# Performance work log

Measured on AMD Instinct MI355X. Metric: run time of the kernel, lower is better.

Reference implementation:

```python
import jax, jax.numpy as jnp
import numpy as np

STRIDES = (8, 16, 32, 64, 128)
SIZES = ((100, 160), (50, 80), (25, 40), (13, 20), (7, 10))  # 800x1280 image, P3-P7
NC = 80      # num_classes
C = 256      # head channels
NCONV = 4    # tower depth
N = 2        # batch
PRIOR_PROB = 0.01


def conv3x3(x, w, b):
    # x: [N,C,H,W], w: [O,I,3,3] -> [N,O,H,W], stride 1, SAME padding
    y = jax.lax.conv_general_dilated(x, w, (1, 1), 'SAME',
                                     dimension_numbers=('NCHW', 'OIHW', 'NCHW'))
    return y + b[None, :, None, None]


def group_norm(x, g, b, groups=32, eps=1e-5):
    n, c, h, w = x.shape
    xr = x.reshape(n, groups, c // groups, h, w)
    m = xr.mean((2, 3, 4), keepdims=True)
    v = ((xr - m) ** 2).mean((2, 3, 4), keepdims=True)
    xn = ((xr - m) * jax.lax.rsqrt(v + eps)).reshape(n, c, h, w)
    return xn * g[None, :, None, None] + b[None, :, None, None]


def setup_inputs() -> dict:
    key = jax.random.key(0)
    ks = iter(jax.random.split(key, 16))
    d = {}
    for l, (h, w) in enumerate(SIZES):
        d[f'feat{l}'] = jax.random.normal(next(ks), (N, C, h, w), jnp.float32)
    # torch init: conv weights ~ N(0, 0.01), biases 0, GN weight 1 / bias 0
    d['cls_w'] = jax.random.normal(next(ks), (NCONV, C, C, 3, 3), jnp.float32) * 0.01
    d['cls_b'] = jnp.zeros((NCONV, C), jnp.float32)
    d['cls_gw'] = jnp.ones((NCONV, C), jnp.float32)
    d['cls_gb'] = jnp.zeros((NCONV, C), jnp.float32)
    d['box_w'] = jax.random.normal(next(ks), (NCONV, C, C, 3, 3), jnp.float32) * 0.01
    d['box_b'] = jnp.zeros((NCONV, C), jnp.float32)
    d['box_gw'] = jnp.ones((NCONV, C), jnp.float32)
    d['box_gb'] = jnp.zeros((NCONV, C), jnp.float32)
    d['score_w'] = jax.random.normal(next(ks), (NC, C, 3, 3), jnp.float32) * 0.01
    bias_value = -np.log((1.0 - PRIOR_PROB) / PRIOR_PROB)
    d['score_b'] = jnp.full((NC,), bias_value, jnp.float32)
    d['pred_w'] = jax.random.normal(next(ks), (4, C, 3, 3), jnp.float32) * 0.01
    d['pred_b'] = jnp.zeros((4,), jnp.float32)
    d['ctr_w'] = jax.random.normal(next(ks), (1, C, 3, 3), jnp.float32) * 0.01
    d['ctr_b'] = jnp.zeros((1,), jnp.float32)
    d['scales'] = jnp.ones((5,), jnp.float32)
    return d


def reference(feat0, feat1, feat2, feat3, feat4,
              cls_w, cls_b, cls_gw, cls_gb,
              box_w, box_b, box_gw, box_gb,
              score_w, score_b, pred_w, pred_b, ctr_w, ctr_b, scales):
    feats = [feat0, feat1, feat2, feat3, feat4]
    outs = []
    for l, x in enumerate(feats):
        c = x
        r = x
        for i in range(NCONV):  # shared cls / bbox towers (conv -> GN -> ReLU)
            c = jax.nn.relu(group_norm(conv3x3(c, cls_w[i], cls_b[i]), cls_gw[i], cls_gb[i]))
            r = jax.nn.relu(group_norm(conv3x3(r, box_w[i], box_b[i]), box_gw[i], box_gb[i]))
        logits = conv3x3(c, score_w, score_b)                     # [N,K,H,W]
        ctr = conv3x3(r, ctr_w, ctr_b)                            # centerness_on_reg=True
        # norm_reg_targets=True: relu(scale * pred) * stride
        reg = jax.nn.relu(conv3x3(r, pred_w, pred_b) * scales[l]) * STRIDES[l]
        n, _, h, w = logits.shape
        logits = logits.transpose(0, 2, 3, 1).reshape(n, h * w, NC)
        ctr = ctr.transpose(0, 2, 3, 1).reshape(n, h * w, 1)
        reg = reg.transpose(0, 2, 3, 1).reshape(n, h * w, 4)
        # ShiftGenerator: grid of (x,y) centers at arange*stride (offset=0)
        sx = jnp.arange(w, dtype=jnp.float32) * STRIDES[l]
        sy = jnp.arange(h, dtype=jnp.float32) * STRIDES[l]
        gy, gx = jnp.meshgrid(sy, sx, indexing='ij')
        shifts = jnp.stack([gx.reshape(-1), gy.reshape(-1)], axis=1)  # [HW,2]
        # Shift2BoxTransform.apply_deltas with weights (1,1,1,1)
        boxes = jnp.concatenate([shifts[None] - reg[..., :2],
                                 shifts[None] + reg[..., 2:]], axis=-1)  # [N,HW,4]
        scores = jax.nn.sigmoid(logits) * jax.nn.sigmoid(ctr)            # [N,HW,K]
        outs.append(jnp.concatenate([scores, boxes], axis=-1))           # [N,HW,K+4]
    return jnp.concatenate(outs, axis=1)  # [N, sum(HW), K+4]
```

## Files before the change

### kernel.cpp

```cpp
#include <hip/hip_runtime.h>
#include <cstddef>

#define NLEV 5
#define TOTROW 21330
#define PTOT 22360

typedef __bf16 bf16x8 __attribute__((ext_vector_type(8)));
typedef float f32x4 __attribute__((ext_vector_type(4)));
typedef unsigned short ushortx8 __attribute__((ext_vector_type(8)));

struct LvlP {
  int tileoff[6];
  int tilesX[5];
  int H[5], W[5];
  int poff[5], pend[5];
  int roff[6];
  float inv8HW[5];
  float strd[5];
};

struct FPtrs { const float* f[5]; };

static __device__ __forceinline__ unsigned short f2bf(float f) {
  union { float f; unsigned u; } v; v.f = f;
  unsigned r = v.u + 0x7fffu + ((v.u >> 16) & 1u);
  return (unsigned short)(r >> 16);
}
static __device__ __forceinline__ float bf2f(unsigned short h) {
  union { unsigned u; float f; } v; v.u = ((unsigned)h) << 16;
  return v.f;
}
static __device__ __forceinline__ int sel5i(const int* a, int l) {
  int v = a[0];
  v = (l == 1) ? a[1] : v; v = (l == 2) ? a[2] : v;
  v = (l == 3) ? a[3] : v; v = (l == 4) ? a[4] : v;
  return v;
}
static __device__ __forceinline__ float sel5f(const float* a, int l) {
  float v = a[0];
  v = (l == 1) ? a[1] : v; v = (l == 2) ? a[2] : v;
  v = (l == 3) ? a[3] : v; v = (l == 4) ? a[4] : v;
  return v;
}

static __device__ __forceinline__ void gload16(const unsigned short* g, unsigned short* l) {
  __builtin_amdgcn_global_load_lds(
      (const __attribute__((address_space(1))) unsigned int*)(const void*)g,
      (__attribute__((address_space(3))) unsigned int*)(void*)l, 16, 0, 0);
}

__global__ __launch_bounds__(256) void to_chlast_all(
    FPtrs F, unsigned short* __restrict__ X, LvlP P)
{
  const int bx = blockIdx.x;
  const int l = (bx >= 250) + (bx >= 313) + (bx >= 329) + (bx >= 334);
  const int boff[5] = {0, 250, 313, 329, 334};
  const int b0 = sel5i(boff, l);
  const int H = sel5i(P.H, l), W = sel5i(P.W, l);
  const int HW = H * W;
  const int poff = sel5i(P.poff, l);
  const float* feat = F.f[l];

  const int n = blockIdx.y >> 2, cb = blockIdx.y & 3;
  const int p0 = (bx - b0) * 64;
  __shared__ unsigned short s[64][72];
  const int t = threadIdx.x;
  const int pl = t & 63, ci = t >> 6;
  const float* src = feat + ((size_t)(n * 256 + cb * 64)) * HW;
#pragma unroll
  for (int i = 0; i < 16; ++i) {
    const int c = ci + i * 4;
    const int p = p0 + pl;
    float v = (p < HW) ? src[(size_t)c * HW + p] : 0.f;
    s[c][pl] = f2bf(v);
  }
  __syncthreads();
  const int cl = t & 63, pi = t >> 6;
#pragma unroll
  for (int i = 0; i < 16; ++i) {
    const int p = p0 + pi + i * 4;
    if (p < HW) {
      const int y = p / W, x = p - y * W;
      const size_t dst = ((size_t)n * PTOT + poff + (y + 1) * (W + 2) + (x + 1)) * 256
                       + cb * 64 + cl;
      X[dst] = s[cl][pi + i * 4];
    }
  }
}

__global__ __launch_bounds__(256) void prep_w(
    const float* __restrict__ cls_w, const float* __restrict__ box_w,
    unsigned short* __restrict__ wtC, unsigned short* __restrict__ wtR,
    const float* __restrict__ sw, const float* __restrict__ sb,
    const float* __restrict__ cw, const float* __restrict__ cbias,
    const float* __restrict__ pw, const float* __restrict__ pb,
    unsigned short* __restrict__ wth, float* __restrict__ bh)
{
  if (blockIdx.x < 9216) {
    const long e = (long)blockIdx.x * 256 + threadIdx.x;
    if (e >= 2359296L) return;
    const int j = (int)(e & 7);
    long r = e >> 3;
    const int oc = (int)(r & 255); r >>= 8;
    const int q = (int)(r & 3); r >>= 2;
    const int tap = (int)(r % 9);
    const long s = r / 9;
    const int ch = (int)(s & 7);
    const int layer = (int)(s >> 3);
    const int ic = ch * 32 + q * 8 + j;
    const long src = (((long)layer * 256 + oc) * 256 + ic) * 9 + tap;
    wtC[e] = f2bf(cls_w[src]);
    wtR[e] = f2bf(box_w[src]);
  } else {
    const long e = (long)(blockIdx.x - 9216) * 256 + threadIdx.x;
    if (e < 589824L) {
      const int j = (int)(e & 7);
      long r = e >> 3;
      const int oc = (int)(r & 127); r >>= 7;
      const int q = (int)(r & 3); r >>= 2;
      const int tap = (int)(r % 9);
      const int ch = (int)(r / 9);
      const int k = ch * 32 + q * 8 + j;
      float v = 0.f;
      if (oc < 80) { if (k < 256) v = sw[((long)(oc * 256 + k)) * 9 + tap]; }
      else if (oc == 80) { if (k >= 256) v = cw[(long)(k - 256) * 9 + tap]; }
      else if (oc < 85) { if (k >= 256) v = pw[((long)((oc - 81) * 256 + (k - 256))) * 9 + tap]; }
      wth[e] = f2bf(v);
    }
    if (blockIdx.x == 9216) {
      const int t = threadIdx.x;
      if (t < 128) bh[t] = (t < 80) ? sb[t] : (t == 80) ? cbias[0] : (t < 85) ? pb[t - 81] : 0.f;
    }
  }
}

__global__ __launch_bounds__(256, 2) void conv_mfma(
    const unsigned short* __restrict__ inC, const unsigned short* __restrict__ inR,
    unsigned short* __restrict__ outC, unsigned short* __restrict__ outR,
    const unsigned short* __restrict__ wtC, const unsigned short* __restrict__ wtR,
    const float* __restrict__ bsC, const float* __restrict__ bsR,
    float* __restrict__ stats, LvlP P, int kimg, int octot)
{
  const int ny = (kimg == 1) ? 4 : 2;
  const int nz = 4;
  const int span = ny * 8;
  const int total = 69 * ny * nz;
  const int SG = total / span;
  const int braw = blockIdx.x;
  int j, yy;
  if (braw < SG * span) {
    j = (braw / span) * 8 + (braw & 7);
    yy = (braw % span) >> 3;
  } else {
    const int p = braw - SG * span;
    const int cpx = (total - SG * span) / ny;
    j = SG * 8 + p % cpx;
    yy = p / cpx;
  }
  const int z = j % nz;
  const int bt = j / nz;
  const int oc0 = yy << 6;

  const int l = (bt >= P.tileoff[1]) + (bt >= P.tileoff[2])
              + (bt >= P.tileoff[3]) + (bt >= P.tileoff[4]);
  const int t = bt - sel5i(P.tileoff, l);
  const int tX = sel5i(P.tilesX, l);
  const int ty = t / tX, tx = t - ty * tX;
  const int x0 = tx << 5, y0 = ty * 12;
  const int H = sel5i(P.H, l), W = sel5i(P.W, l);
  const int W2 = W + 2;
  const int pbase = sel5i(P.poff, l);
  const int pmax = sel5i(P.pend, l) - 1;
  const int rbase = sel5i(P.roff, l);

  const unsigned short *A, *wt;
  const float* bs; unsigned short* out;
  int wchoff = 0;
  if (kimg == 1) {
    const int tower = z >> 1, n = z & 1;
    A = (tower ? inR : inC) + (size_t)n * PTOT * 256;
    wt = tower ? wtR : wtC;
    bs = tower ? bsR : bsC;
    out = (tower ? outR : outC) + (size_t)n * TOTROW * octot;
  } else {
    const int half = z >> 1, n = z & 1;
    A = (half ? inR : inC) + (size_t)n * PTOT * 256;
    wt = wtC; bs = bsC;
    wchoff = half * 8;
    out = outC + (size_t)z * TOTROW * octot;
  }

  __shared__ unsigned short sA[512 * 32];
  __shared__ unsigned short sB[36 * 512];

  const int tid = threadIdx.x;
  const int wv = tid >> 6, lane = tid & 63;
  const int t15 = lane & 15, q = lane >> 4;

  unsigned aoff[8];
#pragma unroll
  for (int it = 0; it < 8; ++it) {
    const int inst = wv + it * 4;
    const int item = (inst << 6) + lane;
    int pos = item >> 2; pos = (pos > 475) ? 475 : pos;
    const int part = item & 3;
    const int hy = pos / 34, hx = pos - hy * 34;
    int pidx = pbase + (y0 + hy) * W2 + (x0 + hx);
    pidx = (pidx > pmax) ? pmax : pidx;
    aoff[it] = ((unsigned)pidx << 8) + (part << 3);
  }

  f32x4 acc[6][4];
#pragma unroll
  for (int g = 0; g < 4; ++g) {
    const float b = bs[oc0 + g * 16 + t15];
#pragma unroll
    for (int f = 0; f < 6; ++f) {
      acc[f][g][0] = b; acc[f][g][1] = b; acc[f][g][2] = b; acc[f][g][3] = b;
    }
  }

  for (int ch = 0; ch < 8; ++ch) {
    const unsigned icb = (unsigned)ch << 5;
    __syncthreads();
#pragma unroll
    for (int it = 0; it < 8; ++it)
      gload16(A + aoff[it] + icb, sA + ((wv + it * 4) << 9));
    const unsigned short* wb = wt + ((size_t)((ch + wchoff) * 36) * octot + oc0) * 8 + (lane << 3);
#pragma unroll
    for (int it = 0; it < 9; ++it)
      gload16(wb + (size_t)(wv + it * 4) * octot * 8, sB + ((wv + it * 4) << 9));
    __syncthreads();

#pragma unroll
    for (int kx = 0; kx < 3; ++kx) {
      bf16x8 af[2][5];
#pragma unroll
      for (int fc = 0; fc < 2; ++fc)
#pragma unroll
        for (int r = 0; r < 5; ++r) {
          const int pos = (wv * 3 + r) * 34 + fc * 16 + t15 + kx;
          af[fc][r] = *(const bf16x8*)(sA + ((pos * 4 + q) << 3));
        }
#pragma unroll
      for (int ky = 0; ky < 3; ++ky) {
        const int tap = ky * 3 + kx;
        bf16x8 b[4];
#pragma unroll
        for (int g = 0; g < 4; ++g)
          b[g] = *(const bf16x8*)(sB + ((((tap * 4 + q) << 6) + g * 16 + t15) << 3));
#pragma unroll
        for (int fr = 0; fr < 3; ++fr)
#pragma unroll
          for (int fc = 0; fc < 2; ++fc) {
            const bf16x8 a = af[fc][fr + ky];
#pragma unroll
            for (int g = 0; g < 4; ++g)
              acc[fr * 2 + fc][g] =
                  __builtin_amdgcn_mfma_f32_16x16x32_bf16(a, b[g], acc[fr * 2 + fc][g], 0, 0, 0);
          }
      }
    }
  }

#pragma unroll
  for (int g = 0; g < 4; ++g) {
    const int oc = oc0 + g * 16 + t15;
    float s = 0.f, ss = 0.f;
#pragma unroll
    for (int f = 0; f < 6; ++f) {
      const int fr = f >> 1, fc = f & 1;
      const int gy = y0 + wv * 3 + fr;
#pragma unroll
      for (int rg = 0; rg < 4; ++rg) {
        const int gx = x0 + fc * 16 + q * 4 + rg;
        if (gy < H && gx < W) {
          const float v = acc[f][g][rg];
          out[(size_t)(rbase + gy * W + gx) * octot + oc] = f2bf(v);
          s += v; ss += v * v;
        }
      }
    }
    if (stats) {
      s += __shfl_xor(s, 1);  ss += __shfl_xor(ss, 1);
      s += __shfl_xor(s, 2);  ss += __shfl_xor(ss, 2);
      s += __shfl_xor(s, 4);  ss += __shfl_xor(ss, 4);
      s += __shfl_xor(s, 16); ss += __shfl_xor(ss, 16);
      if ((lane & 55) == 0) {
        float* st = stats + (((size_t)l * 4 + z) * 32 + (oc >> 3)) * 2;
        atomicAdd(st, s); atomicAdd(st + 1, ss);
      }
    }
  }
}

__global__ __launch_bounds__(256) void gn_apply(
    const unsigned short* __restrict__ Yc, const unsigned short* __restrict__ Yr,
    unsigned short* __restrict__ Xc, unsigned short* __restrict__ Xr,
    const float* __restrict__ stats,
    const float* __restrict__ gwC, const float* __restrict__ gbC,
    const float* __restrict__ gwR, const float* __restrict__ gbR, LvlP P)
{
  const int img = blockIdx.y;
  const int tower = img >> 1, n = img & 1;
  const int e = blockIdx.x * 256 + threadIdx.x;
  const int pos = e >> 5;
  const int g = e & 31;
  if (pos >= TOTROW) return;
  const int l = (pos >= P.roff[1]) + (pos >= P.roff[2]) + (pos >= P.roff[3]) + (pos >= P.roff[4]);
  const int W = sel5i(P.W, l);
  const int local = pos - sel5i(P.roff, l);
  const int y = local / W, x = local - y * W;
  const size_t dst = ((size_t)n * PTOT + sel5i(P.poff, l) + (y + 1) * (W + 2) + (x + 1)) * 256 + g * 8;
  const size_t srco = ((size_t)n * TOTROW + pos) * 256 + g * 8;
  const unsigned short* Y = (tower ? Yr : Yc) + srco;
  unsigned short* X = (tower ? Xr : Xc) + dst;
  const float* gw = (tower ? gwR : gwC) + g * 8;
  const float* gb = (tower ? gbR : gbC) + g * 8;
  const float* st = stats + (((size_t)l * 4 + img) * 32 + g) * 2;
  const float inv = sel5f(P.inv8HW, l);
  const float m = st[0] * inv;
  const float var = st[1] * inv - m * m;
  const float rs = rsqrtf(var + 1e-5f);
  ushortx8 yv = *(const ushortx8*)Y;
  ushortx8 xv;
#pragma unroll
  for (int j = 0; j < 8; ++j) {
    const float yj = bf2f(yv[j]);
    const float v = (yj - m) * rs * gw[j] + gb[j];
    xv[j] = f2bf(fmaxf(v, 0.f));
  }
  *(ushortx8*)X = xv;
}

__global__ __launch_bounds__(256) void head_epi(
    const unsigned short* __restrict__ Yh, float* __restrict__ out,
    const float* __restrict__ scales, LvlP P)
{
  const int n = blockIdx.y;
  const int e = blockIdx.x * 256 + threadIdx.x;
  if (e >= TOTROW * 84) return;
  const int pos = e / 84;
  const int j = e - pos * 84;
  const int l = (pos >= P.roff[1]) + (pos >= P.roff[2]) + (pos >= P.roff[3]) + (pos >= P.roff[4]);
  const unsigned short* yc_ = Yh + ((size_t)n * TOTROW + pos) * 128;
  const unsigned short* yb_ = Yh + ((size_t)(2 + n) * TOTROW + pos) * 128;
  float v;
  if (j < 80) {
    const float lg = bf2f(yc_[j]);
    const float ct = bf2f(yb_[80]);
    v = (1.f / (1.f + __expf(-lg))) * (1.f / (1.f + __expf(-ct)));
  } else {
    const int d = j - 80;
    const float stride = sel5f(P.strd, l);
    const int W = sel5i(P.W, l);
    const int local = pos - sel5i(P.roff, l);
    const int gy = local / W, gx = local - gy * W;
    const float pv = bf2f(yb_[81 + d]);
    const float rg = fmaxf(pv * scales[l], 0.f) * stride;
    const float sx = gx * stride, sy = gy * stride;
    v = (d == 0) ? sx - rg : (d == 1) ? sy - rg : (d == 2) ? sx + rg : sy + rg;
  }
  out[((size_t)n * TOTROW + pos) * 84 + j] = v;
}

extern "C" void kernel_launch(void* const* d_in, const int* in_sizes, int n_in,
                              void* d_out, int out_size, void* d_ws, size_t ws_size,
                              hipStream_t stream)
{
  (void)in_sizes; (void)n_in; (void)out_size; (void)ws_size;

  FPtrs F;
  for (int l = 0; l < 5; ++l) F.f[l] = (const float*)d_in[l];
  const float* cls_w  = (const float*)d_in[5];
  const float* cls_b  = (const float*)d_in[6];
  const float* cls_gw = (const float*)d_in[7];
  const float* cls_gb = (const float*)d_in[8];
  const float* box_w  = (const float*)d_in[9];
  const float* box_b  = (const float*)d_in[10];
  const float* box_gw = (const float*)d_in[11];
  const float* box_gb = (const float*)d_in[12];
  const float* score_w = (const float*)d_in[13];
  const float* score_b = (const float*)d_in[14];
  const float* pred_w  = (const float*)d_in[15];
  const float* pred_b  = (const float*)d_in[16];
  const float* ctr_w   = (const float*)d_in[17];
  const float* ctr_b   = (const float*)d_in[18];
  const float* scales  = (const float*)d_in[19];
  float* out = (float*)d_out;

  static const int Hs[5] = {100, 50, 25, 13, 7};
  static const int Ws[5] = {160, 80, 40, 20, 10};
  LvlP P;
  {
    static const int to[6] = {0, 45, 60, 66, 68, 69};
    static const int tX[5] = {5, 3, 2, 1, 1};
    static const int po[5] = {0, 16524, 20788, 21922, 22252};
    static const int pe[5] = {16524, 20788, 21922, 22252, 22360};
    static const int ro[6] = {0, 16000, 20000, 21000, 21260, 21330};
    for (int i = 0; i < 6; ++i) { P.tileoff[i] = to[i]; P.roff[i] = ro[i]; }
    for (int i = 0; i < 5; ++i) {
      P.tilesX[i] = tX[i]; P.H[i] = Hs[i]; P.W[i] = Ws[i];
      P.poff[i] = po[i]; P.pend[i] = pe[i];
      P.inv8HW[i] = 1.f / (8.f * Hs[i] * Ws[i]);
      P.strd[i] = (float)(8 << i);
    }
  }

  char* p = (char*)d_ws;
  auto alloc = [&](size_t bytes) {
    char* r = p;
    p += (bytes + 255) & ~(size_t)255;
    return r;
  };
  const size_t XPAD = (size_t)2 * PTOT * 256 * 2;
  const size_t YSZ  = (size_t)2 * TOTROW * 256 * 2;
  unsigned short* Xf  = (unsigned short*)alloc(XPAD);
  unsigned short* Xc  = (unsigned short*)alloc(XPAD);
  unsigned short* Xr  = (unsigned short*)alloc(XPAD);
  unsigned short* Yc  = (unsigned short*)alloc(YSZ);
  unsigned short* Yr  = (unsigned short*)alloc(YSZ);
  unsigned short* Yh  = (unsigned short*)alloc((size_t)4 * TOTROW * 128 * 2);
  unsigned short* wtC = (unsigned short*)alloc(4718592);
  unsigned short* wtR = (unsigned short*)alloc(4718592);
  unsigned short* wth = (unsigned short*)alloc(1179648);
  float* bh    = (float*)alloc(512);
  float* stats = (float*)alloc(4 * 5 * 4 * 32 * 2 * sizeof(float));

  hipMemsetAsync(Xf, 0, XPAD, stream);
  hipMemsetAsync(Xc, 0, XPAD, stream);
  hipMemsetAsync(Xr, 0, XPAD, stream);
  hipMemsetAsync(stats, 0, 4 * 5 * 4 * 32 * 2 * sizeof(float), stream);

  prep_w<<<11520, 256, 0, stream>>>(cls_w, box_w, wtC, wtR,
                                    score_w, score_b, ctr_w, ctr_b,
                                    pred_w, pred_b, wth, bh);
  to_chlast_all<<<dim3(336, 8), 256, 0, stream>>>(F, Xf, P);

  for (int i = 0; i < 4; ++i) {
    const unsigned short* ic_ = (i == 0) ? Xf : Xc;
    const unsigned short* ir_ = (i == 0) ? Xf : Xr;
    float* st = stats + (size_t)i * 5 * 4 * 32 * 2;
    conv_mfma<<<dim3(1104), 256, 0, stream>>>(
        ic_, ir_, Yc, Yr,
        wtC + (size_t)i * 589824, wtR + (size_t)i * 589824,
        cls_b + i * 256, box_b + i * 256, st, P, 1, 256);
    gn_apply<<<dim3((TOTROW * 32 + 255) / 256, 4), 256, 0, stream>>>(
        Yc, Yr, Xc, Xr, st,
        cls_gw + i * 256, cls_gb + i * 256,
        box_gw + i * 256, box_gb + i * 256, P);
  }

  conv_mfma<<<dim3(552), 256, 0, stream>>>(
      Xc, Xr, Yh, nullptr, wth, nullptr, bh, nullptr, nullptr, P, 2, 128);
  head_epi<<<dim3((TOTROW * 84 + 255) / 256, 2), 256, 0, stream>>>(
      Yh, out, scales, P);
}
```

Before: 781.7 us.

## Fuse weight prep, layout transpose and border zeroing into one setup kernel

Merges prep_w, the channel-last transpose and the zero-initialisation into a single launch, split into block ranges. The three full-buffer memsets over the padded activations are replaced by writes that zero only the one-pixel halo border of each level, plus a small stats clear. This removes several launches and most memset traffic. It relies on the interior of Xc/Xr always being fully overwritten before it is read, and the transpose branch contains an odd leftover label.

```diff
diff --git a/kernel.cpp b/kernel.cpp
--- a/kernel.cpp
+++ b/kernel.cpp
@@ -49,55 +49,22 @@
       (__attribute__((address_space(3))) unsigned int*)(void*)l, 16, 0, 0);
 }
 
-__global__ __launch_bounds__(256) void to_chlast_all(
-    FPtrs F, unsigned short* __restrict__ X, LvlP P)
-{
-  const int bx = blockIdx.x;
-  const int l = (bx >= 250) + (bx >= 313) + (bx >= 329) + (bx >= 334);
-  const int boff[5] = {0, 250, 313, 329, 334};
-  const int b0 = sel5i(boff, l);
-  const int H = sel5i(P.H, l), W = sel5i(P.W, l);
-  const int HW = H * W;
-  const int poff = sel5i(P.poff, l);
-  const float* feat = F.f[l];
-
-  const int n = blockIdx.y >> 2, cb = blockIdx.y & 3;
-  const int p0 = (bx - b0) * 64;
-  __shared__ unsigned short s[64][72];
-  const int t = threadIdx.x;
-  const int pl = t & 63, ci = t >> 6;
-  const float* src = feat + ((size_t)(n * 256 + cb * 64)) * HW;
-#pragma unroll
-  for (int i = 0; i < 16; ++i) {
-    const int c = ci + i * 4;
-    const int p = p0 + pl;
-    float v = (p < HW) ? src[(size_t)c * HW + p] : 0.f;
-    s[c][pl] = f2bf(v);
-  }
-  __syncthreads();
-  const int cl = t & 63, pi = t >> 6;
-#pragma unroll
-  for (int i = 0; i < 16; ++i) {
-    const int p = p0 + pi + i * 4;
-    if (p < HW) {
-      const int y = p / W, x = p - y * W;
-      const size_t dst = ((size_t)n * PTOT + poff + (y + 1) * (W + 2) + (x + 1)) * 256
-                       + cb * 64 + cl;
-      X[dst] = s[cl][pi + i * 4];
-    }
-  }
-}
-
-__global__ __launch_bounds__(256) void prep_w(
+__global__ __launch_bounds__(256) void setup_all(
     const float* __restrict__ cls_w, const float* __restrict__ box_w,
     unsigned short* __restrict__ wtC, unsigned short* __restrict__ wtR,
     const float* __restrict__ sw, const float* __restrict__ sb,
     const float* __restrict__ cw, const float* __restrict__ cbias,
     const float* __restrict__ pw, const float* __restrict__ pb,
-    unsigned short* __restrict__ wth, float* __restrict__ bh)
+    unsigned short* __restrict__ wth, float* __restrict__ bh,
+    FPtrs F, unsigned short* __restrict__ Xf,
+    unsigned short* __restrict__ Xc, unsigned short* __restrict__ Xr,
+    float* __restrict__ stats, LvlP P)
 {
-  if (blockIdx.x < 9216) {
-    const long e = (long)blockIdx.x * 256 + threadIdx.x;
+  const int bx = blockIdx.x;
+  const int tid = threadIdx.x;
+
+  if (bx < 9216) {
+    const long e = (long)bx * 256 + tid;
     if (e >= 2359296L) return;
     const int j = (int)(e & 7);
     long r = e >> 3;
@@ -111,8 +78,8 @@
     const long src = (((long)layer * 256 + oc) * 256 + ic) * 9 + tap;
     wtC[e] = f2bf(cls_w[src]);
     wtR[e] = f2bf(box_w[src]);
-  } else {
-    const long e = (long)(blockIdx.x - 9216) * 256 + threadIdx.x;
+  } else if (bx < 11520) {
+    const long e = (long)(bx - 9216) * 256 + tid;
     if (e < 589824L) {
       const int j = (int)(e & 7);
       long r = e >> 3;
@@ -127,10 +94,76 @@
       else if (oc < 85) { if (k >= 256) v = pw[((long)((oc - 81) * 256 + (k - 256))) * 9 + tap]; }
       wth[e] = f2bf(v);
     }
-    if (blockIdx.x == 9216) {
-      const int t = threadIdx.x;
-      if (t < 128) bh[t] = (t < 80) ? sb[t] : (t == 80) ? cbias[0] : (t < 85) ? pb[t - 81] : 0.f;
-    }
+    if (bx == 9216 && tid < 128)
+      bh[tid] = (tid < 80) ? sb[tid] : (tid == 80) ? cbias[0] : (tid < 85) ? pb[tid - 81] : 0.f;
+  } else if (bx < 14208) {
+    const int b2 = bx - 11520;
+    const int iy = b2 / 336;
+    const int bx336 = b2 - iy * 336;
+    const int l = (bx336 >= 250) + (bx336 >= 313) + (bx336 >= 329) + (bx336 >= 334);
+    const int boff[5] = {0, 250, 313, 329, 334};
+    const int b0 = sel5i(boff, l);
+    const int H = sel5i(P.H, l), W = sel5i(P.W, l);
+    const int HW = H * W;
+    const int poff = sel5i(P.poff, l);
+    const float* feat = F.f[l];
+
+    const int n = iy >> 2, cb = iy & 3;
+    const int p0 = (bx336 - b0) * 64;
+    __shared__ unsigned short s[64][72];
+    const int pl = tid & 63, ci = tid >> 6;
+    const float* src = feat + ((size_t)(n * 256 + cb * 64)) * HW;
+#pragma unroll
+    for (int i = 0; i < 16; ++i) {
+      const int c = ci + i * 4;
+      const int p = p0 + pl;
+      float v = (p < HW) ? src[(size_t)c * HW + p] : 0.f;
+      s[c][pl] = f2bf(v);
+    }
+    __syncthreads();
+    const int cl = tid & 63, pi = tid >> 6;
+#pragma unroll
+    for (int i = 0; i < 16; ++i) {
+      const int p = p0 + pi + i * 4;
+      if (p < HW) {
+        const int y = p / W, x = p - y * W;
+        const size_t dst = ((size_t)n * PTOT + poff + (y + 1) * (W + 2) + (x + 1)) * 256
+                         + cb * 64 + cl;
+        X_write: ;
+        unsigned short* Xb = Xf;
+        Xb[dst] = s[cl][pi + i * 4];
+      }
+    }
+  } else if (bx < 14981) {
+    const int item = (bx - 14208) * 8 + (tid >> 5);
+    if (item >= 6180) return;
+    const int buf = item / 2060;
+    const int r1 = item - buf * 2060;
+    const int img = r1 / 1030;
+    const int bidx = r1 - img * 1030;
+    static const int cum[5] = {0, 524, 788, 922, 992};
+    const int l = (bidx >= 524) + (bidx >= 788) + (bidx >= 922) + (bidx >= 992);
+    const int b = bidx - sel5i(cum, l);
+    const int H = sel5i(P.H, l), W = sel5i(P.W, l);
+    const int W2 = W + 2;
+    const int poff = sel5i(P.poff, l);
+    int pos;
+    if (b < W2) pos = poff + b;
+    else if (b < 2 * W2) pos = poff + (H + 1) * W2 + (b - W2);
+    else {
+      const int c = b - 2 * W2;
+      const int y = 1 + (c >> 1);
+      const int x = (c & 1) ? (W + 1) : 0;
+      pos = poff + y * W2 + x;
+    }
+    unsigned short* Xb = (buf == 0) ? Xf : (buf == 1) ? Xc : Xr;
+    ushortx8 z8;
+#pragma unroll
+    for (int jj = 0; jj < 8; ++jj) z8[jj] = 0;
+    *(ushortx8*)(Xb + ((size_t)img * PTOT + pos) * 256 + (tid & 31) * 8) = z8;
+  } else {
+    const int e = (bx - 14981) * 256 + tid;
+    if (e < 5120) stats[e] = 0.f;
   }
 }
 
@@ -427,15 +460,10 @@
   float* bh    = (float*)alloc(512);
   float* stats = (float*)alloc(4 * 5 * 4 * 32 * 2 * sizeof(float));
 
-  hipMemsetAsync(Xf, 0, XPAD, stream);
-  hipMemsetAsync(Xc, 0, XPAD, stream);
-  hipMemsetAsync(Xr, 0, XPAD, stream);
-  hipMemsetAsync(stats, 0, 4 * 5 * 4 * 32 * 2 * sizeof(float), stream);
-
-  prep_w<<<11520, 256, 0, stream>>>(cls_w, box_w, wtC, wtR,
-                                    score_w, score_b, ctr_w, ctr_b,
-                                    pred_w, pred_b, wth, bh);
-  to_chlast_all<<<dim3(336, 8), 256, 0, stream>>>(F, Xf, P);
+  setup_all<<<15001, 256, 0, stream>>>(cls_w, box_w, wtC, wtR,
+                                       score_w, score_b, ctr_w, ctr_b,
+                                       pred_w, pred_b, wth, bh,
+                                       F, Xf, Xc, Xr, stats, P);
 
   for (int i = 0; i < 4; ++i) {
     const unsigned short* ic_ = (i == 0) ? Xf : Xc;
```

New measurement: 745.5 us. -4.6%, faster.
